# Kernel tuning notes

Hardware: AMD Instinct MI355X
Metric: run time of the kernel (lower is better)

The kernel has to match this reference:

```python
import jax, jax.numpy as jnp
import numpy as np

DECAY = 0.9    # LIF membrane decay
THRESH = 1.0   # firing threshold


def spike(x):
    # Heaviside spike (forward only)
    return (x > 0).astype(x.dtype)


def setup_inputs() -> dict:
    key = jax.random.key(0)
    k0, k1, k2, k3, k4 = jax.random.split(key, 5)
    B, D, H, O = 4096, 256, 512, 2
    x = jax.random.normal(k0, (B, D), dtype=jnp.float32)
    # torch.nn.Linear-style scaled init
    W1 = jax.random.normal(k1, (H, D), dtype=jnp.float32) * (1.0 / np.sqrt(D))
    b1 = jax.random.normal(k2, (H,), dtype=jnp.float32) * (1.0 / np.sqrt(D))
    W2 = jax.random.normal(k3, (O, H), dtype=jnp.float32) * (1.0 / np.sqrt(H))
    b2 = jax.random.normal(k4, (O,), dtype=jnp.float32) * (1.0 / np.sqrt(H))
    return {"x": x, "W1": W1, "b1": b1, "W2": W2, "b2": b2, "time_steps": 100}


def reference(x, W1, b1, W2, b2, time_steps):
    # Input is identical at every timestep, so fc1 can be hoisted out of the loop.
    h1 = x @ W1.T + b1                         # [B, H]
    B = x.shape[0]
    O = W2.shape[0]

    def step(carry, _):
        mem1, out_spikes = carry
        mem1 = DECAY * mem1 + h1               # leaky integrate
        s1 = spike(mem1 - THRESH)              # fire
        mem1 = mem1 - s1 * THRESH              # soft reset
        h2 = s1 @ W2.T + b2                    # [B, O]
        s2 = spike(h2)
        return (mem1, out_spikes + s2), None

    init = (jnp.zeros_like(h1), jnp.zeros((B, O), dtype=x.dtype))
    (mem1, out_spikes), _ = jax.lax.scan(step, init, None, length=time_steps)
    return out_spikes / time_steps
```

## Files before the change

### kernel.cpp

```cpp
#include <hip/hip_runtime.h>


template <int CTRL>
__device__ __forceinline__ float dpp_add(float v) {
    int x = __builtin_amdgcn_update_dpp(0, __builtin_bit_cast(int, v),
                                        CTRL, 0xF, 0xF, false);
    return v + __builtin_bit_cast(float, x);
}

#define TM 64
#define TN 64
#define TK 64
#define XS_STRIDE4 17
#define WS_STRIDE  68

__global__ __launch_bounds__(256)
__attribute__((amdgpu_waves_per_eu(2, 4)))
void snn_fc1_kernel(const float* __restrict__ x,
                    const float* __restrict__ W1,
                    const float* __restrict__ b1,
                    float* __restrict__ h1ws)
{
    __shared__ float4 xs4[TM * XS_STRIDE4];
    __shared__ float  wsf[TK * WS_STRIDE];

    const int tid  = threadIdx.x;
    const int row0 = blockIdx.x * TM;
    const int col0 = blockIdx.y * TN;

    const int tx = tid & 15;
    const int ty = tid >> 4;

    float acc[4][4];
    {
        const float4 bv = ((const float4*)b1)[(col0 >> 2) + tx];
        #pragma unroll
        for (int r = 0; r < 4; ++r) {
            acc[r][0] = bv.x; acc[r][1] = bv.y;
            acc[r][2] = bv.z; acc[r][3] = bv.w;
        }
    }

    const float4* xg = (const float4*)x;
    const float4* wg = (const float4*)W1;

    for (int chunk = 0; chunk < 4; ++chunk) {
        const int k0q = chunk * 16;

        #pragma unroll
        for (int i = 0; i < 4; ++i) {
            const int idx = tid + i * 256;
            const int row = idx >> 4;
            const int q   = idx & 15;
            xs4[row * XS_STRIDE4 + q] =
                xg[(size_t)(row0 + row) * 64 + k0q + q];
        }
        #pragma unroll
        for (int i = 0; i < 4; ++i) {
            const int idx = tid + i * 256;
            const int q   = idx & 15;
            const int c   = idx >> 4;
            const float4 wv4 = wg[(size_t)(col0 + c) * 64 + k0q + q];
            wsf[(q * 4 + 0) * WS_STRIDE + c] = wv4.x;
            wsf[(q * 4 + 1) * WS_STRIDE + c] = wv4.y;
            wsf[(q * 4 + 2) * WS_STRIDE + c] = wv4.z;
            wsf[(q * 4 + 3) * WS_STRIDE + c] = wv4.w;
        }
        __syncthreads();

        #pragma unroll
        for (int k4 = 0; k4 < 16; ++k4) {
            float4 xv[4], wv[4];
            #pragma unroll
            for (int r = 0; r < 4; ++r)
                xv[r] = xs4[(ty * 4 + r) * XS_STRIDE4 + k4];
            #pragma unroll
            for (int kk = 0; kk < 4; ++kk)
                wv[kk] = *(const float4*)&wsf[(k4 * 4 + kk) * WS_STRIDE + tx * 4];
            #pragma unroll
            for (int kk = 0; kk < 4; ++kk) {
                const float xk0 = xv[0][kk], xk1 = xv[1][kk];
                const float xk2 = xv[2][kk], xk3 = xv[3][kk];
                #pragma unroll
                for (int cc = 0; cc < 4; ++cc) {
                    const float w = wv[kk][cc];
                    acc[0][cc] = fmaf(xk0, w, acc[0][cc]);
                    acc[1][cc] = fmaf(xk1, w, acc[1][cc]);
                    acc[2][cc] = fmaf(xk2, w, acc[2][cc]);
                    acc[3][cc] = fmaf(xk3, w, acc[3][cc]);
                }
            }
        }
        __syncthreads();
    }

    #pragma unroll
    for (int r = 0; r < 4; ++r) {
        float4* dst = (float4*)&h1ws[(size_t)(row0 + ty * 4 + r) * 512
                                     + col0 + tx * 4];
        *dst = make_float4(acc[r][0], acc[r][1], acc[r][2], acc[r][3]);
    }
}

#define DEAD_CUT 0.0999f

template <int E>
__device__ __forceinline__ void lif_body(const float2* __restrict__ cl, int l,
                                         const float* __restrict__ W2,
                                         float bb0, float bb1, int T,
                                         float* __restrict__ dst)
{
    float hv[E], w0r[E], w1r[E], mem[E];
    #pragma unroll
    for (int j = 0; j < E; ++j) {
        const float2 p = cl[j * 64 + l];
        hv[j] = p.x;
        const int idx = __float_as_int(p.y);
        w0r[j] = W2[idx];
        w1r[j] = W2[512 + idx];
        mem[j] = 0.0f;
    }
    float c0 = 0.0f, c1 = 0.0f;
    for (int t = 0; t < T; ++t) {
        float a0 = 0.0f, a1 = 0.0f, a0b = 0.0f, a1b = 0.0f;
        #pragma unroll
        for (int j = 0; j < E; ++j) {
            const float m = __fadd_rn(__fmul_rn(0.9f, mem[j]), hv[j]);
            const float s = (m > 1.0f) ? 1.0f : 0.0f;
            mem[j] = m - s;
            if ((j & 1) == 0) { a0  = fmaf(s, w0r[j], a0);  a1  = fmaf(s, w1r[j], a1);  }
            else              { a0b = fmaf(s, w0r[j], a0b); a1b = fmaf(s, w1r[j], a1b); }
        }
        a0 += a0b; a1 += a1b;
        a0 = dpp_add<0x121>(a0); a1 = dpp_add<0x121>(a1);
        a0 = dpp_add<0x122>(a0); a1 = dpp_add<0x122>(a1);
        a0 = dpp_add<0x124>(a0); a1 = dpp_add<0x124>(a1);
        a0 = dpp_add<0x128>(a0); a1 = dpp_add<0x128>(a1);
        a0 = dpp_add<0x142>(a0); a1 = dpp_add<0x142>(a1);
        a0 = dpp_add<0x143>(a0); a1 = dpp_add<0x143>(a1);
        c0 += ((a0 + bb0) > 0.0f) ? 1.0f : 0.0f;
        c1 += ((a1 + bb1) > 0.0f) ? 1.0f : 0.0f;
    }
    if (l == 48) {
        const float ft = (float)T;
        *(float2*)dst = make_float2(c0 / ft, c1 / ft);
    }
}

__global__ __launch_bounds__(256)
__attribute__((amdgpu_waves_per_eu(4, 4)))
void snn_lif_kernel(const float* __restrict__ h1ws,
                    const float* __restrict__ W2,
                    const float* __restrict__ b2,
                    const int* __restrict__ tsp,
                    float* __restrict__ out)
{
    __shared__ float2 comp[4][512];

    const int tid = threadIdx.x;
    const int l   = tid & 63;
    const int wid = tid >> 6;
    const int row = blockIdx.x * 4 + wid;

    #pragma unroll
    for (int j = 0; j < 8; ++j)
        comp[wid][j * 64 + l] = make_float2(0.0f, __int_as_float(0));

    const float* hrow = h1ws + (size_t)row * 512;
    unsigned base = 0;
    #pragma unroll
    for (int j = 0; j < 8; ++j) {
        const int h = j * 64 + l;
        const float v = hrow[h];
        const bool live = v > DEAD_CUT;
        const unsigned long long m = __ballot(live);
        const unsigned pos = (unsigned)__popcll(m & ((1ull << l) - 1ull));
        if (live) comp[wid][base + pos] = make_float2(v, __int_as_float(h));
        base += (unsigned)__popcll(m);
    }
    __syncthreads();

    const float bb0 = b2[0], bb1 = b2[1];
    const int   T   = tsp[0];
    float* dst = out + (size_t)row * 2;

    int trips = (int)((base + 63u) >> 6);
    if (trips < 1) trips = 1;
    const float2* cl = comp[wid];

    switch (trips) {
        case 1: lif_body<1>(cl, l, W2, bb0, bb1, T, dst); break;
        case 2: lif_body<2>(cl, l, W2, bb0, bb1, T, dst); break;
        case 3: lif_body<3>(cl, l, W2, bb0, bb1, T, dst); break;
        case 4: lif_body<4>(cl, l, W2, bb0, bb1, T, dst); break;
        case 5: lif_body<5>(cl, l, W2, bb0, bb1, T, dst); break;
        case 6: lif_body<6>(cl, l, W2, bb0, bb1, T, dst); break;
        case 7: lif_body<7>(cl, l, W2, bb0, bb1, T, dst); break;
        default: lif_body<8>(cl, l, W2, bb0, bb1, T, dst); break;
    }
}

#define BM 16
#define LDS_H_STRIDE 520

__global__ __launch_bounds__(256, 1) void snn_fused_kernel(
    const float* __restrict__ x, const float* __restrict__ W1,
    const float* __restrict__ b1, const float* __restrict__ W2,
    const float* __restrict__ b2, const int* __restrict__ tsp,
    float* __restrict__ out)
{
    __shared__ float xs[BM * 256];
    __shared__ float h1s[BM * LDS_H_STRIDE];

    const int tid  = threadIdx.x;
    const int row0 = blockIdx.x * BM;

    {
        const float4* xg  = (const float4*)(x + (size_t)row0 * 256);
        float4*       xsv = (float4*)xs;
        #pragma unroll
        for (int i = 0; i < 4; ++i)
            xsv[i * 256 + tid] = xg[i * 256 + tid];
    }
    __syncthreads();

    {
        const int h0 = tid * 2;
        float acc0[BM], acc1[BM];
        const float bia0 = b1[h0], bia1 = b1[h0 + 1];
        #pragma unroll
        for (int b = 0; b < BM; ++b) { acc0[b] = bia0; acc1[b] = bia1; }
        const float4* w0v = (const float4*)(W1 + (size_t)h0 * 256);
        const float4* w1v = (const float4*)(W1 + (size_t)(h0 + 1) * 256);
        const float4* xsv = (const float4*)xs;
        float4 wa = w0v[0], wb = w1v[0];
        #pragma unroll 1
        for (int k4 = 0; k4 < 64; ++k4) {
            const int kn = (k4 < 63) ? k4 + 1 : 63;
            float4 wan = w0v[kn], wbn = w1v[kn];
            float4 xv[BM];
            #pragma unroll
            for (int b = 0; b < BM; ++b) xv[b] = xsv[b * 64 + k4];
            #pragma unroll
            for (int b = 0; b < BM; ++b) {
                acc0[b] = fmaf(xv[b].x, wa.x, acc0[b]);
                acc0[b] = fmaf(xv[b].y, wa.y, acc0[b]);
                acc0[b] = fmaf(xv[b].z, wa.z, acc0[b]);
                acc0[b] = fmaf(xv[b].w, wa.w, acc0[b]);
                acc1[b] = fmaf(xv[b].x, wb.x, acc1[b]);
                acc1[b] = fmaf(xv[b].y, wb.y, acc1[b]);
                acc1[b] = fmaf(xv[b].z, wb.z, acc1[b]);
                acc1[b] = fmaf(xv[b].w, wb.w, acc1[b]);
            }
            wa = wan; wb = wbn;
        }
        #pragma unroll
        for (int b = 0; b < BM; ++b) {
            float2* dst = (float2*)&h1s[b * LDS_H_STRIDE + h0];
            *dst = make_float2(acc0[b], acc1[b]);
        }
    }
    __syncthreads();

    {
        const int l   = tid & 63;
        const int w   = tid >> 6;
        const int l15 = l & 15;
        const int b_local = w * 4 + (l >> 4);
        const int row = row0 + b_local;

        float hv[32], w0r[32], w1r[32], mem[32];
        #pragma unroll
        for (int j = 0; j < 32; ++j) {
            const int h = l15 + j * 16;
            hv[j]  = h1s[b_local * LDS_H_STRIDE + h];
            w0r[j] = W2[h];
            w1r[j] = W2[512 + h];
            mem[j] = 0.0f;
        }
        const float bb0 = b2[0], bb1 = b2[1];
        const int   T   = tsp[0];

        float c0 = 0.0f, c1 = 0.0f;
        for (int t = 0; t < T; ++t) {
            float a0 = 0.0f, a1 = 0.0f, a0b = 0.0f, a1b = 0.0f;
            #pragma unroll
            for (int j = 0; j < 32; j += 2) {
                float m0 = __fadd_rn(__fmul_rn(0.9f, mem[j]),     hv[j]);
                float m1 = __fadd_rn(__fmul_rn(0.9f, mem[j + 1]), hv[j + 1]);
                float s0 = (m0 > 1.0f) ? 1.0f : 0.0f;
                float s1 = (m1 > 1.0f) ? 1.0f : 0.0f;
                mem[j]     = m0 - s0;
                mem[j + 1] = m1 - s1;
                a0  = fmaf(s0, w0r[j],     a0);
                a1  = fmaf(s0, w1r[j],     a1);
                a0b = fmaf(s1, w0r[j + 1], a0b);
                a1b = fmaf(s1, w1r[j + 1], a1b);
            }
            a0 += a0b; a1 += a1b;
            a0 = dpp_add<0x121>(a0); a1 = dpp_add<0x121>(a1);
            a0 = dpp_add<0x122>(a0); a1 = dpp_add<0x122>(a1);
            a0 = dpp_add<0x124>(a0); a1 = dpp_add<0x124>(a1);
            a0 = dpp_add<0x128>(a0); a1 = dpp_add<0x128>(a1);
            c0 += ((a0 + bb0) > 0.0f) ? 1.0f : 0.0f;
            c1 += ((a1 + bb1) > 0.0f) ? 1.0f : 0.0f;
        }

        if (l15 == 0) {
            const float ft = (float)T;
            float2* dst = (float2*)(out + (size_t)row * 2);
            *dst = make_float2(c0 / ft, c1 / ft);
        }
    }
}

extern "C" void kernel_launch(void* const* d_in, const int* in_sizes, int n_in,
                              void* d_out, int out_size, void* d_ws, size_t ws_size,
                              hipStream_t stream) {
    const float* x   = (const float*)d_in[0];
    const float* W1  = (const float*)d_in[1];
    const float* b1  = (const float*)d_in[2];
    const float* W2  = (const float*)d_in[3];
    const float* b2  = (const float*)d_in[4];
    const int*   tsp = (const int*)d_in[5];
    float*       out = (float*)d_out;

    const int B = in_sizes[0] / 256;
    const size_t need = (size_t)B * 512 * sizeof(float);

    if (ws_size >= need) {
        float* h1ws = (float*)d_ws;
        snn_fc1_kernel<<<dim3(B / TM, 512 / TN), dim3(256), 0, stream>>>(
            x, W1, b1, h1ws);
        snn_lif_kernel<<<dim3(B / 4), dim3(256), 0, stream>>>(
            h1ws, W2, b2, tsp, out);
    } else {
        snn_fused_kernel<<<dim3(B / BM), dim3(256), 0, stream>>>(
            x, W1, b1, W2, b2, tsp, out);
    }
}
```

Baseline: 69.51 us.

## Split each LIF wave into two half-waves, one batch row each

The LIF kernel now gives each 64-lane wave two batch rows, one per 32-lane half. Each row's live neurons are compacted into its own LDS list, and the block covers 8 rows instead of 4. This cuts wasted padding lanes when the live-neuron count is not a multiple of 64, and drops the last cross-row DPP reduction step. In exchange, unrolled loop bodies get longer (up to 16 entries), register pressure rises with relaxed waves-per-EU, and the cross-half DPP reduction must keep the two rows' sums separate to stay correct.

```diff
diff --git a/kernel.cpp b/kernel.cpp
--- a/kernel.cpp
+++ b/kernel.cpp
@@ -105,15 +105,15 @@
 #define DEAD_CUT 0.0999f
 
 template <int E>
-__device__ __forceinline__ void lif_body(const float2* __restrict__ cl, int l,
-                                         const float* __restrict__ W2,
-                                         float bb0, float bb1, int T,
-                                         float* __restrict__ dst)
+__device__ __forceinline__ void lif_body2(const float2* __restrict__ cl, int l31,
+                                          const float* __restrict__ W2,
+                                          float bb0, float bb1, int T,
+                                          float* __restrict__ dst, bool writer)
 {
     float hv[E], w0r[E], w1r[E], mem[E];
     #pragma unroll
     for (int j = 0; j < E; ++j) {
-        const float2 p = cl[j * 64 + l];
+        const float2 p = cl[j * 32 + l31];
         hv[j] = p.x;
         const int idx = __float_as_int(p.y);
         w0r[j] = W2[idx];
@@ -137,66 +137,82 @@
         a0 = dpp_add<0x124>(a0); a1 = dpp_add<0x124>(a1);
         a0 = dpp_add<0x128>(a0); a1 = dpp_add<0x128>(a1);
         a0 = dpp_add<0x142>(a0); a1 = dpp_add<0x142>(a1);
-        a0 = dpp_add<0x143>(a0); a1 = dpp_add<0x143>(a1);
         c0 += ((a0 + bb0) > 0.0f) ? 1.0f : 0.0f;
         c1 += ((a1 + bb1) > 0.0f) ? 1.0f : 0.0f;
     }
-    if (l == 48) {
+    if (writer) {
         const float ft = (float)T;
         *(float2*)dst = make_float2(c0 / ft, c1 / ft);
     }
 }
 
 __global__ __launch_bounds__(256)
-__attribute__((amdgpu_waves_per_eu(4, 4)))
+__attribute__((amdgpu_waves_per_eu(2, 4)))
 void snn_lif_kernel(const float* __restrict__ h1ws,
                     const float* __restrict__ W2,
                     const float* __restrict__ b2,
                     const int* __restrict__ tsp,
                     float* __restrict__ out)
 {
-    __shared__ float2 comp[4][512];
-
-    const int tid = threadIdx.x;
-    const int l   = tid & 63;
-    const int wid = tid >> 6;
-    const int row = blockIdx.x * 4 + wid;
-
+    __shared__ float2 comp[8][512];
+
+    const int tid  = threadIdx.x;
+    const int l    = tid & 63;
+    const int wid  = tid >> 6;
+    const int half = l >> 5;
+    const int l31  = l & 31;
+    const int rowA = blockIdx.x * 8 + wid * 2;
+
+    unsigned bases[2];
     #pragma unroll
-    for (int j = 0; j < 8; ++j)
-        comp[wid][j * 64 + l] = make_float2(0.0f, __int_as_float(0));
-
-    const float* hrow = h1ws + (size_t)row * 512;
-    unsigned base = 0;
-    #pragma unroll
-    for (int j = 0; j < 8; ++j) {
-        const int h = j * 64 + l;
-        const float v = hrow[h];
-        const bool live = v > DEAD_CUT;
-        const unsigned long long m = __ballot(live);
-        const unsigned pos = (unsigned)__popcll(m & ((1ull << l) - 1ull));
-        if (live) comp[wid][base + pos] = make_float2(v, __int_as_float(h));
-        base += (unsigned)__popcll(m);
-    }
-    __syncthreads();
+    for (int r = 0; r < 2; ++r) {
+        float2* cw = comp[wid * 2 + r];
+        #pragma unroll
+        for (int j = 0; j < 8; ++j)
+            cw[j * 64 + l] = make_float2(0.0f, __int_as_float(0));
+        const float* hrow = h1ws + (size_t)(rowA + r) * 512;
+        unsigned base = 0;
+        #pragma unroll
+        for (int j = 0; j < 8; ++j) {
+            const int h = j * 64 + l;
+            const float v = hrow[h];
+            const bool live = v > DEAD_CUT;
+            const unsigned long long m = __ballot(live);
+            const unsigned pos = (unsigned)__popcll(m & ((1ull << l) - 1ull));
+            if (live) cw[base + pos] = make_float2(v, __int_as_float(h));
+            base += (unsigned)__popcll(m);
+        }
+        bases[r] = base;
+    }
 
     const float bb0 = b2[0], bb1 = b2[1];
     const int   T   = tsp[0];
+    const int   row = rowA + half;
     float* dst = out + (size_t)row * 2;
-
-    int trips = (int)((base + 63u) >> 6);
+    const bool writer = (l31 == 16);
+
+    const unsigned mx = bases[0] > bases[1] ? bases[0] : bases[1];
+    int trips = (int)((mx + 31u) >> 5);
     if (trips < 1) trips = 1;
-    const float2* cl = comp[wid];
+    const float2* cl = comp[wid * 2 + half];
 
     switch (trips) {
-        case 1: lif_body<1>(cl, l, W2, bb0, bb1, T, dst); break;
-        case 2: lif_body<2>(cl, l, W2, bb0, bb1, T, dst); break;
-        case 3: lif_body<3>(cl, l, W2, bb0, bb1, T, dst); break;
-        case 4: lif_body<4>(cl, l, W2, bb0, bb1, T, dst); break;
-        case 5: lif_body<5>(cl, l, W2, bb0, bb1, T, dst); break;
-        case 6: lif_body<6>(cl, l, W2, bb0, bb1, T, dst); break;
-        case 7: lif_body<7>(cl, l, W2, bb0, bb1, T, dst); break;
-        default: lif_body<8>(cl, l, W2, bb0, bb1, T, dst); break;
+        case 1:  lif_body2<1>(cl, l31, W2, bb0, bb1, T, dst, writer); break;
+        case 2:  lif_body2<2>(cl, l31, W2, bb0, bb1, T, dst, writer); break;
+        case 3:  lif_body2<3>(cl, l31, W2, bb0, bb1, T, dst, writer); break;
+        case 4:  lif_body2<4>(cl, l31, W2, bb0, bb1, T, dst, writer); break;
+        case 5:  lif_body2<5>(cl, l31, W2, bb0, bb1, T, dst, writer); break;
+        case 6:  lif_body2<6>(cl, l31, W2, bb0, bb1, T, dst, writer); break;
+        case 7:  lif_body2<7>(cl, l31, W2, bb0, bb1, T, dst, writer); break;
+        case 8:  lif_body2<8>(cl, l31, W2, bb0, bb1, T, dst, writer); break;
+        case 9:  lif_body2<9>(cl, l31, W2, bb0, bb1, T, dst, writer); break;
+        case 10: lif_body2<10>(cl, l31, W2, bb0, bb1, T, dst, writer); break;
+        case 11: lif_body2<11>(cl, l31, W2, bb0, bb1, T, dst, writer); break;
+        case 12: lif_body2<12>(cl, l31, W2, bb0, bb1, T, dst, writer); break;
+        case 13: lif_body2<13>(cl, l31, W2, bb0, bb1, T, dst, writer); break;
+        case 14: lif_body2<14>(cl, l31, W2, bb0, bb1, T, dst, writer); break;
+        case 15: lif_body2<15>(cl, l31, W2, bb0, bb1, T, dst, writer); break;
+        default: lif_body2<16>(cl, l31, W2, bb0, bb1, T, dst, writer); break;
     }
 }
 
@@ -332,7 +348,7 @@
         float* h1ws = (float*)d_ws;
         snn_fc1_kernel<<<dim3(B / TM, 512 / TN), dim3(256), 0, stream>>>(
             x, W1, b1, h1ws);
-        snn_lif_kernel<<<dim3(B / 4), dim3(256), 0, stream>>>(
+        snn_lif_kernel<<<dim3(B / 8), dim3(256), 0, stream>>>(
             h1ws, W2, b2, tsp, out);
     } else {
         snn_fused_kernel<<<dim3(B / BM), dim3(256), 0, stream>>>(
```

After: 58.37 us. 16.0% less time.
